# Kernel tuning notes

Measured on AMD Instinct MI355X. Metric: run time of the kernel, lower is better.

The kernel has to match this reference:

```python
import jax, jax.numpy as jnp
import numpy as np
from jax import lax

H, W, C, HIDDEN = 1024, 1024, 16, 128

_SOBEL_X = jnp.array([[-1., 0., 1.], [-2., 0., 2.], [-1., 0., 1.]], dtype=jnp.float32)
_SOBEL_Y = jnp.array([[-1., -2., -1.], [0., 0., 0.], [1., 2., 1.]], dtype=jnp.float32)


def setup_inputs() -> dict:
    key = jax.random.key(0)
    ks = jax.random.split(key, 5)
    state = jax.random.normal(ks[0], (H, W, C), dtype=jnp.float32)
    # 1x1 convs are per-pixel matmuls; expose weights as (out,in) matrices.
    # NOTE: the torch module zero-inits the output layer; we randomize for a
    # non-trivial numerical baseline.
    W1 = jax.random.normal(ks[1], (HIDDEN, 3 * C), dtype=jnp.float32) * 0.1
    b1 = jax.random.normal(ks[2], (HIDDEN,), dtype=jnp.float32) * 0.1
    W2 = jax.random.normal(ks[3], (C, HIDDEN), dtype=jnp.float32) * 0.1
    b2 = jax.random.normal(ks[4], (C,), dtype=jnp.float32) * 0.1
    return {"state": state, "W1": W1, "b1": b1, "W2": W2, "b2": b2}


def _depthwise_circular(x, k2d):
    # x: (1, C, H, W); k2d: (3, 3). Circular pad then VALID depthwise conv
    # (torch Conv2d is cross-correlation, matching lax.conv_general_dilated).
    c = x.shape[1]
    xp = jnp.pad(x, ((0, 0), (0, 0), (1, 1), (1, 1)), mode="wrap")
    kern = jnp.broadcast_to(k2d, (c, 1, 3, 3))  # (O=C, I/groups=1, 3, 3)
    return lax.conv_general_dilated(
        xp, kern, window_strides=(1, 1), padding="VALID",
        dimension_numbers=("NCHW", "OIHW", "NCHW"), feature_group_count=c)


def reference(state, W1, b1, W2, b2):
    # state: (H, W, C) -> (1, C, H, W)
    x = jnp.transpose(state, (2, 0, 1))[None]
    gx = _depthwise_circular(x, _SOBEL_X)
    gy = _depthwise_circular(x, _SOBEL_Y)
    perc = jnp.concatenate([gx, gy, x], axis=1)  # (1, 3C, H, W)
    hidden = jax.nn.relu(
        jnp.einsum("oc,bchw->bohw", W1, perc) + b1[None, :, None, None])
    delta = jnp.einsum("co,bohw->bchw", W2, hidden) + b2[None, :, None, None]
    return jnp.transpose(delta[0], (1, 2, 0))  # (H, W, C)
```

## Files before the change

kernel.cpp:

```cpp
#include <hip/hip_runtime.h>


constexpr int Hc = 1024, Wc = 1024;

typedef __attribute__((ext_vector_type(8))) short short8;
typedef __attribute__((ext_vector_type(4))) float f32x4;
typedef __attribute__((ext_vector_type(2))) unsigned int uint2v;

__device__ __forceinline__ unsigned short bfu(float x) {
    __bf16 b = (__bf16)x;
    return __builtin_bit_cast(unsigned short, b);
}
__device__ __forceinline__ unsigned pack2(float a, float b) {
    return (unsigned)bfu(a) | ((unsigned)bfu(b) << 16);
}

__device__ __forceinline__ void swap32(unsigned x, unsigned y, unsigned& o0, unsigned& o1) {
#if __has_builtin(__builtin_amdgcn_permlane32_swap)
    uint2v r = __builtin_amdgcn_permlane32_swap(x, y, false, false);
    o0 = r[0]; o1 = r[1];
#else
    unsigned xs = (unsigned)__shfl_xor((int)x, 32, 64);
    unsigned ys = (unsigned)__shfl_xor((int)y, 32, 64);
    const bool hi = (threadIdx.x & 32) != 0;
    o0 = hi ? ys : x;
    o1 = hi ? y : xs;
#endif
}
__device__ __forceinline__ void swap16(unsigned a, unsigned b, unsigned& o0, unsigned& o1) {
#if __has_builtin(__builtin_amdgcn_permlane16_swap)
    uint2v r = __builtin_amdgcn_permlane16_swap(a, b, false, false);
    o0 = r[0]; o1 = r[1];
#else
    unsigned as = (unsigned)__shfl_xor((int)a, 16, 64);
    unsigned bs = (unsigned)__shfl_xor((int)b, 16, 64);
    const bool hi = (threadIdx.x & 16) != 0;
    o0 = hi ? bs : a;
    o1 = hi ? b : as;
#endif
}

__global__ __launch_bounds__(256) void nca_prep(
    const float* __restrict__ W1c, const float* __restrict__ b1c,
    const float* __restrict__ W2c,
    unsigned short* __restrict__ ws1, unsigned short* __restrict__ ws2)
{
    const int u = blockIdx.x * 256 + threadIdx.x;
    if (u < 128 * 160) {
        const int row = u / 160, k = u - row * 160;
        const int pos = k >> 4, c = k & 15;
        float v;
        if (pos < 9) {
            const int dy = pos / 3, dx = pos - dy * 3;
            v = (float)((dx - 1) * (1 + (dy == 1))) * W1c[row * 48 + c]
              + (float)((dy - 1) * (1 + (dx == 1))) * W1c[row * 48 + 16 + c];
            if (pos == 4) v += W1c[row * 48 + 32 + c];
        } else {
            v = (k == 144) ? b1c[row] : 0.f;
        }
        ws1[row * 168 + k] = bfu(v);
    } else if (u < 128 * 160 + 16 * 128) {
        const int w = u - 128 * 160;
        ws2[w] = bfu(W2c[w]);
    }
}

template <bool USE_WS>
__global__ __launch_bounds__(256, 2) void nca_main(
    const float* __restrict__ state,
    const float* __restrict__ W1c, const float* __restrict__ b1c,
    const float* __restrict__ W2c, const float* __restrict__ b2c,
    const unsigned short* __restrict__ ws1,
    const unsigned short* __restrict__ ws2,
    float* __restrict__ out)
{
    __shared__ short w1f[128 * 168];
    __shared__ short tile[6 * 66 * 24];

    const int tid  = threadIdx.x;
    const int lane = tid & 63;
    const int wv   = tid >> 6;
    const int p    = lane & 15;
    const int g    = lane >> 4;

    const int r0 = (blockIdx.x >> 4) << 2;
    const int c0 = (blockIdx.x & 15) << 6;

    if (USE_WS) {
        #pragma unroll
        for (int it = 0; it < 11; ++it) {
            const int chunk = it * 4 + wv;
            if (chunk < 42) {
                const int off = chunk * 1024;
                __builtin_amdgcn_global_load_lds(
                    (const __attribute__((address_space(1))) unsigned int*)
                        ((const char*)ws1 + off + lane * 16),
                    (__attribute__((address_space(3))) unsigned int*)
                        ((char*)w1f + off),
                    16, 0, 0);
            }
        }
    } else {
        for (int u = tid; u < 128 * 160; u += 256) {
            const int row = u / 160, k = u - row * 160;
            const int pos = k >> 4, c = k & 15;
            float v;
            if (pos < 9) {
                const int dy = pos / 3, dx = pos - dy * 3;
                v = (float)((dx - 1) * (1 + (dy == 1))) * W1c[row * 48 + c]
                  + (float)((dy - 1) * (1 + (dx == 1))) * W1c[row * 48 + 16 + c];
                if (pos == 4) v += W1c[row * 48 + 32 + c];
            } else {
                v = (k == 144) ? b1c[row] : 0.f;
            }
            w1f[row * 168 + k] = (short)bfu(v);
        }
    }

    for (int u = tid; u < 6 * 66 * 4; u += 256) {
        const int q = u & 3;
        const int pidx = u >> 2;
        const int tr = pidx / 66, tc = pidx - tr * 66;
        const int sr = (r0 - 1 + tr) & (Hc - 1);
        const int sc = (c0 - 1 + tc) & (Wc - 1);
        const float4 f = *reinterpret_cast<const float4*>(
            state + (((sr << 10) + sc) << 4) + 4 * q);
        uint2 pk; pk.x = pack2(f.x, f.y); pk.y = pack2(f.z, f.w);
        *reinterpret_cast<uint2*>(&tile[pidx * 24 + 4 * q]) = pk;
    }

    __syncthreads();

    short8 w2f[4];
    if (USE_WS) {
        const unsigned short* wsp = ws2 + p * 128 + 8 * g;
        #pragma unroll
        for (int kc = 0; kc < 4; ++kc)
            w2f[kc] = *reinterpret_cast<const short8*>(wsp + 32 * kc);
    } else {
        #pragma unroll
        for (int kc = 0; kc < 4; ++kc) {
            const float* qp = W2c + p * 128 + 32 * kc + 8 * g;
            const float4 A = *reinterpret_cast<const float4*>(qp);
            const float4 B = *reinterpret_cast<const float4*>(qp + 4);
            uint4 uu{pack2(A.x, A.y), pack2(A.z, A.w), pack2(B.x, B.y), pack2(B.z, B.w)};
            w2f[kc] = __builtin_bit_cast(short8, uu);
        }
    }

    int baddr[5];
    #pragma unroll
    for (int i = 0; i < 5; ++i) {
        int j = 4 * i + g; if (j > 17) j = 17;
        const int pos = j >> 1, ch = j & 1;
        const int dy = pos / 3, dx = pos - dy * 3;
        baddr[i] = ((wv + dy) * 66 + p + dx) * 24 + 8 * ch;
    }
    short8 b1f[4][5];
    #pragma unroll
    for (int pt = 0; pt < 4; ++pt) {
        #pragma unroll
        for (int i = 0; i < 4; ++i)
            b1f[pt][i] = *reinterpret_cast<const short8*>(&tile[baddr[i] + pt * 384]);
        short8 v;
        if (g < 2) {
            v = *reinterpret_cast<const short8*>(&tile[baddr[4] + pt * 384]);
        } else if (g == 2) {
            uint4 uu{0x3F80u, 0u, 0u, 0u};
            v = __builtin_bit_cast(short8, uu);
        } else {
            uint4 uu{0u, 0u, 0u, 0u};
            v = __builtin_bit_cast(short8, uu);
        }
        b1f[pt][4] = v;
    }

    f32x4 acc2[4];
    {
        const float4 bv = *reinterpret_cast<const float4*>(b2c + 4 * g);
        #pragma unroll
        for (int pt = 0; pt < 4; ++pt) {
            acc2[pt][0] = bv.x; acc2[pt][1] = bv.y; acc2[pt][2] = bv.z; acc2[pt][3] = bv.w;
        }
    }

    const int abase = p * 168 + 8 * g;
    #pragma unroll
    for (int kc2 = 0; kc2 < 4; ++kc2) {
        f32x4 aa[4], ab[4];
        #pragma unroll
        for (int pt = 0; pt < 4; ++pt) {
            aa[pt] = (f32x4){0.f, 0.f, 0.f, 0.f};
            ab[pt] = (f32x4){0.f, 0.f, 0.f, 0.f};
        }
        #pragma unroll
        for (int i = 0; i < 5; ++i) {
            const short8 A = *reinterpret_cast<const short8*>(
                &w1f[abase + (2 * kc2) * 2688 + 32 * i]);
            #pragma unroll
            for (int pt = 0; pt < 4; ++pt)
                aa[pt] = __builtin_amdgcn_mfma_f32_16x16x32_bf16(A, b1f[pt][i], aa[pt], 0, 0, 0);
        }
        #pragma unroll
        for (int i = 0; i < 5; ++i) {
            const short8 A = *reinterpret_cast<const short8*>(
                &w1f[abase + (2 * kc2 + 1) * 2688 + 32 * i]);
            #pragma unroll
            for (int pt = 0; pt < 4; ++pt)
                ab[pt] = __builtin_amdgcn_mfma_f32_16x16x32_bf16(A, b1f[pt][i], ab[pt], 0, 0, 0);
        }
        #pragma unroll
        for (int pt = 0; pt < 4; ++pt) {
            const unsigned Pa0 = pack2(fmaxf(aa[pt][0], 0.f), fmaxf(aa[pt][1], 0.f));
            const unsigned Pa1 = pack2(fmaxf(aa[pt][2], 0.f), fmaxf(aa[pt][3], 0.f));
            const unsigned Pb0 = pack2(fmaxf(ab[pt][0], 0.f), fmaxf(ab[pt][1], 0.f));
            const unsigned Pb1 = pack2(fmaxf(ab[pt][2], 0.f), fmaxf(ab[pt][3], 0.f));
            unsigned s0, s1, t0, t1, r0_, r1_, r2_, r3_;
            swap32(Pa0, Pb0, s0, s1);
            swap16(s0, s1, r0_, r2_);
            swap32(Pa1, Pb1, t0, t1);
            swap16(t0, t1, r1_, r3_);
            uint4 uu{r0_, r1_, r2_, r3_};
            const short8 hb = __builtin_bit_cast(short8, uu);
            acc2[pt] = __builtin_amdgcn_mfma_f32_16x16x32_bf16(w2f[kc2], hb, acc2[pt], 0, 0, 0);
        }
    }

    const int orow = r0 + wv;
    #pragma unroll
    for (int pt = 0; pt < 4; ++pt) {
        const int pix = (orow << 10) + c0 + 16 * pt + p;
        float4 o; o.x = acc2[pt][0]; o.y = acc2[pt][1]; o.z = acc2[pt][2]; o.w = acc2[pt][3];
        *reinterpret_cast<float4*>(out + (pix << 4) + 4 * g) = o;
    }
}

extern "C" void kernel_launch(void* const* d_in, const int* in_sizes, int n_in,
                              void* d_out, int out_size, void* d_ws, size_t ws_size,
                              hipStream_t stream) {
    const float* state = (const float*)d_in[0];
    const float* W1c   = (const float*)d_in[1];
    const float* b1c   = (const float*)d_in[2];
    const float* W2c   = (const float*)d_in[3];
    const float* b2c   = (const float*)d_in[4];
    float* out = (float*)d_out;

    unsigned short* ws1 = (unsigned short*)d_ws;
    unsigned short* ws2 = ws1 + 128 * 168;
    const size_t ws_needed = (size_t)(128 * 168 + 16 * 128) * sizeof(unsigned short);

    if (ws_size >= ws_needed) {
        nca_prep<<<88, 256, 0, stream>>>(W1c, b1c, W2c, ws1, ws2);
        nca_main<true><<<4096, 256, 0, stream>>>(state, W1c, b1c, W2c, b2c, ws1, ws2, out);
    } else {
        nca_main<false><<<4096, 256, 0, stream>>>(state, W1c, b1c, W2c, b2c, ws1, ws2, out);
    }
}
```

Baseline: 71.99 us.

## Make blocks persistent over 32 rows with double-buffered state tile prefetch

Each block now handles 8 consecutive 4-row strips (512 blocks instead of 4096), so the 43KB W1 staging in LDS is paid once per block instead of once per strip. The next strip's state rows are prefetched into registers during the current strip's MFMA work and written into a second LDS tile buffer. The loop order is also restructured: W1 fragments are held in registers per half and B operands are read from LDS per pixel tile. The costs are higher register pressure, an extra LDS buffer that may reduce occupancy, and only 512 blocks to spread across the CUs.

```diff
diff --git a/kernel.cpp b/kernel.cpp
--- a/kernel.cpp
+++ b/kernel.cpp
@@ -75,7 +75,7 @@
     float* __restrict__ out)
 {
     __shared__ short w1f[128 * 168];
-    __shared__ short tile[6 * 66 * 24];
+    __shared__ short tile[2][6 * 66 * 24];
 
     const int tid  = threadIdx.x;
     const int lane = tid & 63;
@@ -83,7 +83,7 @@
     const int p    = lane & 15;
     const int g    = lane >> 4;
 
-    const int r0 = (blockIdx.x >> 4) << 2;
+    const int r0 = (blockIdx.x >> 4) << 5;
     const int c0 = (blockIdx.x & 15) << 6;
 
     if (USE_WS) {
@@ -117,19 +117,18 @@
         }
     }
 
-    for (int u = tid; u < 6 * 66 * 4; u += 256) {
-        const int q = u & 3;
-        const int pidx = u >> 2;
-        const int tr = pidx / 66, tc = pidx - tr * 66;
-        const int sr = (r0 - 1 + tr) & (Hc - 1);
-        const int sc = (c0 - 1 + tc) & (Wc - 1);
-        const float4 f = *reinterpret_cast<const float4*>(
-            state + (((sr << 10) + sc) << 4) + 4 * q);
-        uint2 pk; pk.x = pack2(f.x, f.y); pk.y = pack2(f.z, f.w);
-        *reinterpret_cast<uint2*>(&tile[pidx * 24 + 4 * q]) = pk;
-    }
-
-    __syncthreads();
+    const int q = tid & 3;
+    int str_[7], sgofs[7], slofs[7];
+    #pragma unroll
+    for (int s = 0; s < 7; ++s) {
+        const int pidx = (tid >> 2) + 64 * s;
+        const int tr = pidx / 66;
+        const int tc = pidx - tr * 66;
+        str_[s]  = tr;
+        sgofs[s] = (((c0 - 1 + tc) & (Wc - 1)) << 6) + (q << 4);
+        slofs[s] = pidx * 48 + (q << 3);
+    }
+    const bool has7 = (tid < 48);
 
     short8 w2f[4];
     if (USE_WS) {
@@ -147,6 +146,7 @@
             w2f[kc] = __builtin_bit_cast(short8, uu);
         }
     }
+    const float4 bv = *reinterpret_cast<const float4*>(b2c + 4 * g);
 
     int baddr[5];
     #pragma unroll
@@ -156,82 +156,134 @@
         const int dy = pos / 3, dx = pos - dy * 3;
         baddr[i] = ((wv + dy) * 66 + p + dx) * 24 + 8 * ch;
     }
-    short8 b1f[4][5];
+    const int abase = p * 168 + 8 * g;
+
+    int ocol[4];
     #pragma unroll
-    for (int pt = 0; pt < 4; ++pt) {
-        #pragma unroll
-        for (int i = 0; i < 4; ++i)
-            b1f[pt][i] = *reinterpret_cast<const short8*>(&tile[baddr[i] + pt * 384]);
-        short8 v;
-        if (g < 2) {
-            v = *reinterpret_cast<const short8*>(&tile[baddr[4] + pt * 384]);
-        } else if (g == 2) {
-            uint4 uu{0x3F80u, 0u, 0u, 0u};
-            v = __builtin_bit_cast(short8, uu);
-        } else {
-            uint4 uu{0u, 0u, 0u, 0u};
-            v = __builtin_bit_cast(short8, uu);
-        }
-        b1f[pt][4] = v;
-    }
-
-    f32x4 acc2[4];
+    for (int pt = 0; pt < 4; ++pt) ocol[pt] = ((c0 + 16 * pt + p) << 6) + (g << 4);
+
+    const char* stby = (const char*)state;
+    char* outby = (char*)out;
+
     {
-        const float4 bv = *reinterpret_cast<const float4*>(b2c + 4 * g);
+        float4 sreg[7];
+        const int rb = r0 - 1;
+        #pragma unroll
+        for (int s = 0; s < 7; ++s) {
+            if (s < 6 || has7) {
+                const long sr = (long)((rb + str_[s]) & (Hc - 1));
+                sreg[s] = *reinterpret_cast<const float4*>(stby + (sr << 16) + sgofs[s]);
+            }
+        }
+        short* wb = &tile[0][0];
+        #pragma unroll
+        for (int s = 0; s < 7; ++s) {
+            if (s < 6 || has7) {
+                uint2 pk; pk.x = pack2(sreg[s].x, sreg[s].y); pk.y = pack2(sreg[s].z, sreg[s].w);
+                *reinterpret_cast<uint2*>((char*)wb + slofs[s]) = pk;
+            }
+        }
+    }
+    __syncthreads();
+
+    #pragma unroll 2
+    for (int t = 0; t < 8; ++t) {
+        float4 sreg[7];
+        if (t < 7) {
+            const int rb = r0 + 4 * (t + 1) - 1;
+            #pragma unroll
+            for (int s = 0; s < 7; ++s) {
+                if (s < 6 || has7) {
+                    const long sr = (long)((rb + str_[s]) & (Hc - 1));
+                    sreg[s] = *reinterpret_cast<const float4*>(stby + (sr << 16) + sgofs[s]);
+                }
+            }
+        }
+
+        const short* tb = &tile[t & 1][0];
+        f32x4 acc2[4];
         #pragma unroll
         for (int pt = 0; pt < 4; ++pt) {
             acc2[pt][0] = bv.x; acc2[pt][1] = bv.y; acc2[pt][2] = bv.z; acc2[pt][3] = bv.w;
         }
-    }
-
-    const int abase = p * 168 + 8 * g;
-    #pragma unroll
-    for (int kc2 = 0; kc2 < 4; ++kc2) {
-        f32x4 aa[4], ab[4];
+
+        #pragma unroll
+        for (int half = 0; half < 2; ++half) {
+            short8 Ar[4][5];
+            #pragma unroll
+            for (int tt = 0; tt < 4; ++tt) {
+                #pragma unroll
+                for (int i = 0; i < 5; ++i) {
+                    Ar[tt][i] = *reinterpret_cast<const short8*>(
+                        &w1f[abase + (64 * half + 16 * tt) * 168 + 32 * i]);
+                }
+            }
+
+            #pragma unroll
+            for (int pt = 0; pt < 4; ++pt) {
+                f32x4 h[4];
+                #pragma unroll
+                for (int tt = 0; tt < 4; ++tt) h[tt] = (f32x4){0.f, 0.f, 0.f, 0.f};
+
+                #pragma unroll
+                for (int i = 0; i < 5; ++i) {
+                    short8 B;
+                    if (i < 4) {
+                        B = *reinterpret_cast<const short8*>(&tb[baddr[i] + pt * 384]);
+                    } else {
+                        if (g < 2) {
+                            B = *reinterpret_cast<const short8*>(&tb[baddr[4] + pt * 384]);
+                        } else if (g == 2) {
+                            uint4 uu{0x3F80u, 0u, 0u, 0u};
+                            B = __builtin_bit_cast(short8, uu);
+                        } else {
+                            uint4 uu{0u, 0u, 0u, 0u};
+                            B = __builtin_bit_cast(short8, uu);
+                        }
+                    }
+                    #pragma unroll
+                    for (int tt = 0; tt < 4; ++tt)
+                        h[tt] = __builtin_amdgcn_mfma_f32_16x16x32_bf16(Ar[tt][i], B, h[tt], 0, 0, 0);
+                }
+
+                #pragma unroll
+                for (int pr = 0; pr < 2; ++pr) {
+                    const f32x4 ha = h[2 * pr], hc = h[2 * pr + 1];
+                    const unsigned Pa0 = pack2(fmaxf(ha[0], 0.f), fmaxf(ha[1], 0.f));
+                    const unsigned Pa1 = pack2(fmaxf(ha[2], 0.f), fmaxf(ha[3], 0.f));
+                    const unsigned Pb0 = pack2(fmaxf(hc[0], 0.f), fmaxf(hc[1], 0.f));
+                    const unsigned Pb1 = pack2(fmaxf(hc[2], 0.f), fmaxf(hc[3], 0.f));
+                    unsigned s0, s1, t0, t1, u0, u1, u2, u3;
+                    swap32(Pa0, Pb0, s0, s1);
+                    swap16(s0, s1, u0, u2);
+                    swap32(Pa1, Pb1, t0, t1);
+                    swap16(t0, t1, u1, u3);
+                    uint4 uu{u0, u1, u2, u3};
+                    const short8 hbf = __builtin_bit_cast(short8, uu);
+                    acc2[pt] = __builtin_amdgcn_mfma_f32_16x16x32_bf16(
+                        w2f[2 * half + pr], hbf, acc2[pt], 0, 0, 0);
+                }
+            }
+        }
+
+        const long orow = (long)(r0 + 4 * t + wv) << 16;
         #pragma unroll
         for (int pt = 0; pt < 4; ++pt) {
-            aa[pt] = (f32x4){0.f, 0.f, 0.f, 0.f};
-            ab[pt] = (f32x4){0.f, 0.f, 0.f, 0.f};
-        }
-        #pragma unroll
-        for (int i = 0; i < 5; ++i) {
-            const short8 A = *reinterpret_cast<const short8*>(
-                &w1f[abase + (2 * kc2) * 2688 + 32 * i]);
+            float4 o; o.x = acc2[pt][0]; o.y = acc2[pt][1]; o.z = acc2[pt][2]; o.w = acc2[pt][3];
+            *reinterpret_cast<float4*>(outby + orow + ocol[pt]) = o;
+        }
+
+        if (t < 7) {
+            short* wb = &tile[(t + 1) & 1][0];
             #pragma unroll
-            for (int pt = 0; pt < 4; ++pt)
-                aa[pt] = __builtin_amdgcn_mfma_f32_16x16x32_bf16(A, b1f[pt][i], aa[pt], 0, 0, 0);
-        }
-        #pragma unroll
-        for (int i = 0; i < 5; ++i) {
-            const short8 A = *reinterpret_cast<const short8*>(
-                &w1f[abase + (2 * kc2 + 1) * 2688 + 32 * i]);
-            #pragma unroll
-            for (int pt = 0; pt < 4; ++pt)
-                ab[pt] = __builtin_amdgcn_mfma_f32_16x16x32_bf16(A, b1f[pt][i], ab[pt], 0, 0, 0);
-        }
-        #pragma unroll
-        for (int pt = 0; pt < 4; ++pt) {
-            const unsigned Pa0 = pack2(fmaxf(aa[pt][0], 0.f), fmaxf(aa[pt][1], 0.f));
-            const unsigned Pa1 = pack2(fmaxf(aa[pt][2], 0.f), fmaxf(aa[pt][3], 0.f));
-            const unsigned Pb0 = pack2(fmaxf(ab[pt][0], 0.f), fmaxf(ab[pt][1], 0.f));
-            const unsigned Pb1 = pack2(fmaxf(ab[pt][2], 0.f), fmaxf(ab[pt][3], 0.f));
-            unsigned s0, s1, t0, t1, r0_, r1_, r2_, r3_;
-            swap32(Pa0, Pb0, s0, s1);
-            swap16(s0, s1, r0_, r2_);
-            swap32(Pa1, Pb1, t0, t1);
-            swap16(t0, t1, r1_, r3_);
-            uint4 uu{r0_, r1_, r2_, r3_};
-            const short8 hb = __builtin_bit_cast(short8, uu);
-            acc2[pt] = __builtin_amdgcn_mfma_f32_16x16x32_bf16(w2f[kc2], hb, acc2[pt], 0, 0, 0);
-        }
-    }
-
-    const int orow = r0 + wv;
-    #pragma unroll
-    for (int pt = 0; pt < 4; ++pt) {
-        const int pix = (orow << 10) + c0 + 16 * pt + p;
-        float4 o; o.x = acc2[pt][0]; o.y = acc2[pt][1]; o.z = acc2[pt][2]; o.w = acc2[pt][3];
-        *reinterpret_cast<float4*>(out + (pix << 4) + 4 * g) = o;
+            for (int s = 0; s < 7; ++s) {
+                if (s < 6 || has7) {
+                    uint2 pk; pk.x = pack2(sreg[s].x, sreg[s].y); pk.y = pack2(sreg[s].z, sreg[s].w);
+                    *reinterpret_cast<uint2*>((char*)wb + slofs[s]) = pk;
+                }
+            }
+        }
+        __syncthreads();
     }
 }
 
@@ -251,8 +303,8 @@
 
     if (ws_size >= ws_needed) {
         nca_prep<<<88, 256, 0, stream>>>(W1c, b1c, W2c, ws1, ws2);
-        nca_main<true><<<4096, 256, 0, stream>>>(state, W1c, b1c, W2c, b2c, ws1, ws2, out);
+        nca_main<true><<<512, 256, 0, stream>>>(state, W1c, b1c, W2c, b2c, ws1, ws2, out);
     } else {
-        nca_main<false><<<4096, 256, 0, stream>>>(state, W1c, b1c, W2c, b2c, ws1, ws2, out);
-    }
-}
+        nca_main<false><<<512, 256, 0, stream>>>(state, W1c, b1c, W2c, b2c, ws1, ws2, out);
+    }
+}
```

Result: faster. 65.45 us (-9.1%).

## Load stencil inputs directly from global, enlarge block tile, shrink weight LDS stride

Applied to the files above, without the earlier changes.

Drops the shared-memory input tile and has each lane gather its 3x3 stencil neighbours straight from global memory (through cache), converting to bf16 in registers. Each block now loops over 16 rows instead of 4, so the W1 LDS load is amortised over four times as many pixels, and the grid falls from 4096 to 1024 blocks. The LDS weight row stride drops from 168 to 152 to cut LDS use, occupancy is raised to 3 blocks per CU, and the block index is swizzled for locality. The cost is roughly nine redundant global reads per pixel that rely on L1/L2 hits, plus more address arithmetic.

```diff
diff --git a/kernel.cpp b/kernel.cpp
--- a/kernel.cpp
+++ b/kernel.cpp
@@ -2,6 +2,8 @@
 
 
 constexpr int Hc = 1024, Wc = 1024;
+constexpr int W1S = 152;
+constexpr int W1PAD = 19968;
 
 typedef __attribute__((ext_vector_type(8))) short short8;
 typedef __attribute__((ext_vector_type(4))) float f32x4;
@@ -46,27 +48,29 @@
     unsigned short* __restrict__ ws1, unsigned short* __restrict__ ws2)
 {
     const int u = blockIdx.x * 256 + threadIdx.x;
-    if (u < 128 * 160) {
-        const int row = u / 160, k = u - row * 160;
-        const int pos = k >> 4, c = k & 15;
-        float v;
-        if (pos < 9) {
-            const int dy = pos / 3, dx = pos - dy * 3;
-            v = (float)((dx - 1) * (1 + (dy == 1))) * W1c[row * 48 + c]
-              + (float)((dy - 1) * (1 + (dx == 1))) * W1c[row * 48 + 16 + c];
-            if (pos == 4) v += W1c[row * 48 + 32 + c];
-        } else {
-            v = (k == 144) ? b1c[row] : 0.f;
-        }
-        ws1[row * 168 + k] = bfu(v);
-    } else if (u < 128 * 160 + 16 * 128) {
-        const int w = u - 128 * 160;
+    if (u < W1PAD) {
+        const int row = u / W1S, k = u - row * W1S;
+        float v = 0.f;
+        if (row < 128) {
+            if (k < 144) {
+                const int pos = k >> 4, c = k & 15;
+                const int dy = pos / 3, dx = pos - dy * 3;
+                v = (float)((dx - 1) * (1 + (dy == 1))) * W1c[row * 48 + c]
+                  + (float)((dy - 1) * (1 + (dx == 1))) * W1c[row * 48 + 16 + c];
+                if (pos == 4) v += W1c[row * 48 + 32 + c];
+            } else if (k == 144) {
+                v = b1c[row];
+            }
+        }
+        ws1[u] = bfu(v);
+    } else if (u < W1PAD + 16 * 128) {
+        const int w = u - W1PAD;
         ws2[w] = bfu(W2c[w]);
     }
 }
 
 template <bool USE_WS>
-__global__ __launch_bounds__(256, 2) void nca_main(
+__global__ __launch_bounds__(256, 3) void nca_main(
     const float* __restrict__ state,
     const float* __restrict__ W1c, const float* __restrict__ b1c,
     const float* __restrict__ W2c, const float* __restrict__ b2c,
@@ -74,8 +78,7 @@
     const unsigned short* __restrict__ ws2,
     float* __restrict__ out)
 {
-    __shared__ short w1f[128 * 168];
-    __shared__ short tile[6 * 66 * 24];
+    __shared__ short w1f[W1PAD];
 
     const int tid  = threadIdx.x;
     const int lane = tid & 63;
@@ -83,14 +86,16 @@
     const int p    = lane & 15;
     const int g    = lane >> 4;
 
-    const int r0 = (blockIdx.x >> 4) << 2;
-    const int c0 = (blockIdx.x & 15) << 6;
+    int bid = (int)blockIdx.x;
+    bid = ((bid & 7) << 7) | (bid >> 3);
+    const int r0 = (bid >> 4) << 4;
+    const int c0 = (bid & 15) << 6;
 
     if (USE_WS) {
         #pragma unroll
-        for (int it = 0; it < 11; ++it) {
+        for (int it = 0; it < 10; ++it) {
             const int chunk = it * 4 + wv;
-            if (chunk < 42) {
+            if (chunk < 39) {
                 const int off = chunk * 1024;
                 __builtin_amdgcn_global_load_lds(
                     (const __attribute__((address_space(1))) unsigned int*)
@@ -101,35 +106,43 @@
             }
         }
     } else {
-        for (int u = tid; u < 128 * 160; u += 256) {
-            const int row = u / 160, k = u - row * 160;
-            const int pos = k >> 4, c = k & 15;
-            float v;
-            if (pos < 9) {
-                const int dy = pos / 3, dx = pos - dy * 3;
-                v = (float)((dx - 1) * (1 + (dy == 1))) * W1c[row * 48 + c]
-                  + (float)((dy - 1) * (1 + (dx == 1))) * W1c[row * 48 + 16 + c];
-                if (pos == 4) v += W1c[row * 48 + 32 + c];
-            } else {
-                v = (k == 144) ? b1c[row] : 0.f;
-            }
-            w1f[row * 168 + k] = (short)bfu(v);
-        }
-    }
-
-    for (int u = tid; u < 6 * 66 * 4; u += 256) {
-        const int q = u & 3;
-        const int pidx = u >> 2;
-        const int tr = pidx / 66, tc = pidx - tr * 66;
-        const int sr = (r0 - 1 + tr) & (Hc - 1);
-        const int sc = (c0 - 1 + tc) & (Wc - 1);
-        const float4 f = *reinterpret_cast<const float4*>(
-            state + (((sr << 10) + sc) << 4) + 4 * q);
-        uint2 pk; pk.x = pack2(f.x, f.y); pk.y = pack2(f.z, f.w);
-        *reinterpret_cast<uint2*>(&tile[pidx * 24 + 4 * q]) = pk;
-    }
-
-    __syncthreads();
+        for (int u = tid; u < W1PAD; u += 256) {
+            const int row = u / W1S, k = u - row * W1S;
+            float v = 0.f;
+            if (row < 128) {
+                if (k < 144) {
+                    const int pos = k >> 4, c = k & 15;
+                    const int dy = pos / 3, dx = pos - dy * 3;
+                    v = (float)((dx - 1) * (1 + (dy == 1))) * W1c[row * 48 + c]
+                      + (float)((dy - 1) * (1 + (dx == 1))) * W1c[row * 48 + 16 + c];
+                    if (pos == 4) v += W1c[row * 48 + 32 + c];
+                } else if (k == 144) {
+                    v = b1c[row];
+                }
+            }
+            w1f[u] = (short)bfu(v);
+        }
+    }
+
+    const int gb = g & 1;
+    unsigned colpk[10] = {0, 0, 0, 0, 0, 0, 0, 0, 0, 0};
+    unsigned dypk = 0;
+    {
+        const int cbase = c0 - 1 + p;
+        #pragma unroll
+        for (int i = 0; i < 5; ++i) {
+            const int pos = (i < 4) ? (2 * i + (g >> 1)) : 8;
+            const int dy = pos / 3, dx = pos - 3 * dy;
+            dypk |= (unsigned)dy << (2 * i);
+            #pragma unroll
+            for (int pt = 0; pt < 4; ++pt) {
+                const unsigned cbyte =
+                    ((unsigned)((cbase + dx + 16 * pt) & (Wc - 1)) << 6) | ((unsigned)gb << 5);
+                const int j = pt * 5 + i;
+                colpk[j >> 1] |= cbyte << (16 * (j & 1));
+            }
+        }
+    }
 
     short8 w2f[4];
     if (USE_WS) {
@@ -147,91 +160,112 @@
             w2f[kc] = __builtin_bit_cast(short8, uu);
         }
     }
-
-    int baddr[5];
+    const float4 bv = *reinterpret_cast<const float4*>(b2c + 4 * g);
+
+    int ocol[4];
     #pragma unroll
-    for (int i = 0; i < 5; ++i) {
-        int j = 4 * i + g; if (j > 17) j = 17;
-        const int pos = j >> 1, ch = j & 1;
-        const int dy = pos / 3, dx = pos - dy * 3;
-        baddr[i] = ((wv + dy) * 66 + p + dx) * 24 + 8 * ch;
-    }
-    short8 b1f[4][5];
-    #pragma unroll
-    for (int pt = 0; pt < 4; ++pt) {
-        #pragma unroll
-        for (int i = 0; i < 4; ++i)
-            b1f[pt][i] = *reinterpret_cast<const short8*>(&tile[baddr[i] + pt * 384]);
-        short8 v;
-        if (g < 2) {
-            v = *reinterpret_cast<const short8*>(&tile[baddr[4] + pt * 384]);
-        } else if (g == 2) {
-            uint4 uu{0x3F80u, 0u, 0u, 0u};
-            v = __builtin_bit_cast(short8, uu);
-        } else {
-            uint4 uu{0u, 0u, 0u, 0u};
-            v = __builtin_bit_cast(short8, uu);
-        }
-        b1f[pt][4] = v;
-    }
-
-    f32x4 acc2[4];
-    {
-        const float4 bv = *reinterpret_cast<const float4*>(b2c + 4 * g);
-        #pragma unroll
-        for (int pt = 0; pt < 4; ++pt) {
-            acc2[pt][0] = bv.x; acc2[pt][1] = bv.y; acc2[pt][2] = bv.z; acc2[pt][3] = bv.w;
-        }
-    }
-
-    const int abase = p * 168 + 8 * g;
-    #pragma unroll
-    for (int kc2 = 0; kc2 < 4; ++kc2) {
-        f32x4 aa[4], ab[4];
-        #pragma unroll
-        for (int pt = 0; pt < 4; ++pt) {
-            aa[pt] = (f32x4){0.f, 0.f, 0.f, 0.f};
-            ab[pt] = (f32x4){0.f, 0.f, 0.f, 0.f};
-        }
-        #pragma unroll
-        for (int i = 0; i < 5; ++i) {
-            const short8 A = *reinterpret_cast<const short8*>(
-                &w1f[abase + (2 * kc2) * 2688 + 32 * i]);
-            #pragma unroll
-            for (int pt = 0; pt < 4; ++pt)
-                aa[pt] = __builtin_amdgcn_mfma_f32_16x16x32_bf16(A, b1f[pt][i], aa[pt], 0, 0, 0);
-        }
-        #pragma unroll
-        for (int i = 0; i < 5; ++i) {
-            const short8 A = *reinterpret_cast<const short8*>(
-                &w1f[abase + (2 * kc2 + 1) * 2688 + 32 * i]);
-            #pragma unroll
-            for (int pt = 0; pt < 4; ++pt)
-                ab[pt] = __builtin_amdgcn_mfma_f32_16x16x32_bf16(A, b1f[pt][i], ab[pt], 0, 0, 0);
-        }
-        #pragma unroll
-        for (int pt = 0; pt < 4; ++pt) {
-            const unsigned Pa0 = pack2(fmaxf(aa[pt][0], 0.f), fmaxf(aa[pt][1], 0.f));
-            const unsigned Pa1 = pack2(fmaxf(aa[pt][2], 0.f), fmaxf(aa[pt][3], 0.f));
-            const unsigned Pb0 = pack2(fmaxf(ab[pt][0], 0.f), fmaxf(ab[pt][1], 0.f));
-            const unsigned Pb1 = pack2(fmaxf(ab[pt][2], 0.f), fmaxf(ab[pt][3], 0.f));
-            unsigned s0, s1, t0, t1, r0_, r1_, r2_, r3_;
-            swap32(Pa0, Pb0, s0, s1);
-            swap16(s0, s1, r0_, r2_);
-            swap32(Pa1, Pb1, t0, t1);
-            swap16(t0, t1, r1_, r3_);
-            uint4 uu{r0_, r1_, r2_, r3_};
-            const short8 hb = __builtin_bit_cast(short8, uu);
-            acc2[pt] = __builtin_amdgcn_mfma_f32_16x16x32_bf16(w2f[kc2], hb, acc2[pt], 0, 0, 0);
-        }
-    }
-
-    const int orow = r0 + wv;
-    #pragma unroll
-    for (int pt = 0; pt < 4; ++pt) {
-        const int pix = (orow << 10) + c0 + 16 * pt + p;
-        float4 o; o.x = acc2[pt][0]; o.y = acc2[pt][1]; o.z = acc2[pt][2]; o.w = acc2[pt][3];
-        *reinterpret_cast<float4*>(out + (pix << 4) + 4 * g) = o;
+    for (int pt = 0; pt < 4; ++pt) ocol[pt] = ((c0 + 16 * pt + p) << 6) + (g << 4);
+    const int abase = p * W1S + 8 * g;
+
+    const char* stby = (const char*)state;
+    char* outby = (char*)out;
+
+    __syncthreads();
+
+    #pragma unroll 1
+    for (int t = 0; t < 4; ++t) {
+        const int rbase = r0 + 4 * t + wv - 1;
+        unsigned rowb[5];
+        #pragma unroll
+        for (int i = 0; i < 5; ++i)
+            rowb[i] = (unsigned)((rbase + (int)((dypk >> (2 * i)) & 3u)) & (Hc - 1)) << 16;
+
+        const long orow = (long)(r0 + 4 * t + wv) << 16;
+
+        #pragma unroll
+        for (int ptg = 0; ptg < 2; ++ptg) {
+            short8 bf[2][5];
+            #pragma unroll
+            for (int pp = 0; pp < 2; ++pp) {
+                #pragma unroll
+                for (int i = 0; i < 5; ++i) {
+                    const int j = (2 * ptg + pp) * 5 + i;
+                    const unsigned off =
+                        rowb[i] + ((colpk[j >> 1] >> (16 * (j & 1))) & 0xffffu);
+                    if (i < 4) {
+                        const float4 A0 = *reinterpret_cast<const float4*>(stby + off);
+                        const float4 A1 = *reinterpret_cast<const float4*>(stby + off + 16);
+                        uint4 uu{pack2(A0.x, A0.y), pack2(A0.z, A0.w),
+                                 pack2(A1.x, A1.y), pack2(A1.z, A1.w)};
+                        bf[pp][i] = __builtin_bit_cast(short8, uu);
+                    } else {
+                        if (g < 2) {
+                            const float4 A0 = *reinterpret_cast<const float4*>(stby + off);
+                            const float4 A1 = *reinterpret_cast<const float4*>(stby + off + 16);
+                            uint4 uu{pack2(A0.x, A0.y), pack2(A0.z, A0.w),
+                                     pack2(A1.x, A1.y), pack2(A1.z, A1.w)};
+                            bf[pp][i] = __builtin_bit_cast(short8, uu);
+                        } else if (g == 2) {
+                            uint4 uu{0x3F80u, 0u, 0u, 0u};
+                            bf[pp][i] = __builtin_bit_cast(short8, uu);
+                        } else {
+                            uint4 uu{0u, 0u, 0u, 0u};
+                            bf[pp][i] = __builtin_bit_cast(short8, uu);
+                        }
+                    }
+                }
+            }
+
+            f32x4 acc2[2];
+            #pragma unroll
+            for (int pp = 0; pp < 2; ++pp) {
+                acc2[pp][0] = bv.x; acc2[pp][1] = bv.y;
+                acc2[pp][2] = bv.z; acc2[pp][3] = bv.w;
+            }
+
+            #pragma unroll
+            for (int half = 0; half < 2; ++half) {
+                #pragma unroll
+                for (int tg = 0; tg < 2; ++tg) {
+                    short8 Ar0[5], Ar1[5];
+                    const int rofs = abase + (64 * half + 32 * tg) * W1S;
+                    #pragma unroll
+                    for (int i = 0; i < 5; ++i) {
+                        Ar0[i] = *reinterpret_cast<const short8*>(&w1f[rofs + 32 * i]);
+                        Ar1[i] = *reinterpret_cast<const short8*>(&w1f[rofs + 16 * W1S + 32 * i]);
+                    }
+                    #pragma unroll
+                    for (int pp = 0; pp < 2; ++pp) {
+                        f32x4 h0 = {0.f, 0.f, 0.f, 0.f}, h1 = {0.f, 0.f, 0.f, 0.f};
+                        #pragma unroll
+                        for (int i = 0; i < 5; ++i) {
+                            h0 = __builtin_amdgcn_mfma_f32_16x16x32_bf16(Ar0[i], bf[pp][i], h0, 0, 0, 0);
+                            h1 = __builtin_amdgcn_mfma_f32_16x16x32_bf16(Ar1[i], bf[pp][i], h1, 0, 0, 0);
+                        }
+                        const unsigned Pa0 = pack2(fmaxf(h0[0], 0.f), fmaxf(h0[1], 0.f));
+                        const unsigned Pa1 = pack2(fmaxf(h0[2], 0.f), fmaxf(h0[3], 0.f));
+                        const unsigned Pb0 = pack2(fmaxf(h1[0], 0.f), fmaxf(h1[1], 0.f));
+                        const unsigned Pb1 = pack2(fmaxf(h1[2], 0.f), fmaxf(h1[3], 0.f));
+                        unsigned s0, s1, t0, t1, u0, u1, u2, u3;
+                        swap32(Pa0, Pb0, s0, s1);
+                        swap16(s0, s1, u0, u2);
+                        swap32(Pa1, Pb1, t0, t1);
+                        swap16(t0, t1, u1, u3);
+                        uint4 uu{u0, u1, u2, u3};
+                        acc2[pp] = __builtin_amdgcn_mfma_f32_16x16x32_bf16(
+                            w2f[2 * half + tg], __builtin_bit_cast(short8, uu), acc2[pp], 0, 0, 0);
+                    }
+                }
+            }
+
+            #pragma unroll
+            for (int pp = 0; pp < 2; ++pp) {
+                float4 o;
+                o.x = acc2[pp][0]; o.y = acc2[pp][1];
+                o.z = acc2[pp][2]; o.w = acc2[pp][3];
+                *reinterpret_cast<float4*>(outby + orow + ocol[2 * ptg + pp]) = o;
+            }
+        }
     }
 }
 
@@ -246,13 +280,13 @@
     float* out = (float*)d_out;
 
     unsigned short* ws1 = (unsigned short*)d_ws;
-    unsigned short* ws2 = ws1 + 128 * 168;
-    const size_t ws_needed = (size_t)(128 * 168 + 16 * 128) * sizeof(unsigned short);
+    unsigned short* ws2 = ws1 + W1PAD;
+    const size_t ws_needed = (size_t)(W1PAD + 16 * 128) * sizeof(unsigned short);
 
     if (ws_size >= ws_needed) {
-        nca_prep<<<88, 256, 0, stream>>>(W1c, b1c, W2c, ws1, ws2);
-        nca_main<true><<<4096, 256, 0, stream>>>(state, W1c, b1c, W2c, b2c, ws1, ws2, out);
+        nca_prep<<<(W1PAD + 16 * 128 + 255) / 256, 256, 0, stream>>>(W1c, b1c, W2c, ws1, ws2);
+        nca_main<true><<<1024, 256, 0, stream>>>(state, W1c, b1c, W2c, b2c, ws1, ws2, out);
     } else {
-        nca_main<false><<<4096, 256, 0, stream>>>(state, W1c, b1c, W2c, b2c, ws1, ws2, out);
-    }
-}
+        nca_main<false><<<1024, 256, 0, stream>>>(state, W1c, b1c, W2c, b2c, ws1, ws2, out);
+    }
+}
```

Measured after the change: 218.2 us. 203% more time.
